# Optimization experiments

Hardware: AMD Instinct MI355X
Metric: run time of the kernel (lower is better)

## Reference

```python
import jax, jax.numpy as jnp
import numpy as np

N = 100000      # nodes
E = 3200000     # edges (avg degree 32)
F_IN = 512      # num_features
H = 256         # hidden
C = 64          # num_classes
K = 20          # APPNP propagation steps
ALPHA = 0.1     # teleport probability


def setup_inputs() -> dict:
    key = jax.random.key(0)
    k0, k1, k2, k3 = jax.random.split(key, 4)
    x = jax.random.normal(k0, (N, F_IN), dtype=jnp.float32)
    edge_index = jax.random.randint(k1, (2, E), 0, N, dtype=jnp.int64)
    W1 = jax.random.normal(k2, (F_IN, H), dtype=jnp.float32) / np.sqrt(F_IN).astype(np.float32)
    b1 = jnp.zeros((H,), jnp.float32)
    W2 = jax.random.normal(k3, (H, C), dtype=jnp.float32) / np.sqrt(H).astype(np.float32)
    b2 = jnpp = jnp.zeros((C,), jnp.float32)
    return {"x": x, "edge_index": edge_index, "W1": W1, "b1": b1, "W2": W2, "b2": b2}


def reference(x, edge_index, W1, b1, W2, b2):
    n = x.shape[0]
    # MLP encoder (dropout is identity in eval mode)
    h = jax.nn.relu(x @ W1 + b1) @ W2 + b2            # [N, C]

    # gcn_norm with added self-loops (PyG APPNP default)
    self_loop = jnp.arange(n, dtype=edge_index.dtype)
    src = jnp.concatenate([edge_index[0], self_loop])  # message sources
    dst = jnp.concatenate([edge_index[1], self_loop])  # aggregation targets
    deg = jax.ops.segment_sum(jnp.ones_like(dst, jnp.float32), dst, num_segments=n)
    deg_inv_sqrt = jnp.where(deg > 0, jax.lax.rsqrt(deg), 0.0)
    norm = (deg_inv_sqrt[src] * deg_inv_sqrt[dst])[:, None]  # [E+N, 1]

    def prop_step(_, z):
        msg = z[src] * norm                               # gather + scale
        agg = jax.ops.segment_sum(msg, dst, num_segments=n)  # scatter-add
        return (1.0 - ALPHA) * agg + ALPHA * h            # teleport mix

    z = jax.lax.fori_loop(0, K, prop_step, h)
    return jax.nn.log_softmax(z, axis=1)
```

## Files before the change

### kernel.cpp

```cpp
#include <hip/hip_runtime.h>
#include <hip/hip_bf16.h>
#include <math.h>

#define NN 100000
#define EE 3200000
#define FIN 512
#define HID 256
#define CLS 64
#define KST 20

typedef __attribute__((ext_vector_type(8))) short bf16x8;
typedef __attribute__((ext_vector_type(4))) float f32x4;

__device__ __forceinline__ short f2bf(float f) {
    union { __hip_bfloat16 b; short s; } u;
    u.b = __float2bfloat16(f);
    return u.s;
}
__device__ __forceinline__ float bf2f(__hip_bfloat16 b) { return __bfloat162float(b); }
__device__ __forceinline__ float lobf(unsigned u) { return __uint_as_float(u << 16); }
__device__ __forceinline__ float hibf(unsigned u) { return __uint_as_float(u & 0xffff0000u); }
__device__ __forceinline__ unsigned packbf(float lo, float hi) {
    return (unsigned)(unsigned short)f2bf(lo) | ((unsigned)(unsigned short)f2bf(hi) << 16);
}


__global__ void zero_kernel(int* __restrict__ degcnt, int* __restrict__ cursor) {
    int i = blockIdx.x * 256 + threadIdx.x;
    if (i < NN) { degcnt[i] = 0; cursor[i] = 0; }
}

__global__ void count_kernel(const int* __restrict__ edst, int* __restrict__ degcnt) {
    int e = blockIdx.x * 256 + threadIdx.x;
    if (e < EE) atomicAdd(&degcnt[edst[e]], 1);
}

__global__ __launch_bounds__(1024) void scan1_kernel(const int* __restrict__ degcnt,
                                                     int* __restrict__ tmp,
                                                     int* __restrict__ bsum) {
    __shared__ int s[1024];
    int t = threadIdx.x;
    int i = blockIdx.x * 1024 + t;
    int v = (i < NN) ? degcnt[i] : 0;
    s[t] = v;
    __syncthreads();
    for (int off = 1; off < 1024; off <<= 1) {
        int xv = (t >= off) ? s[t - off] : 0;
        __syncthreads();
        s[t] += xv;
        __syncthreads();
    }
    if (i < NN) tmp[i] = s[t] - v;
    if (t == 1023) bsum[blockIdx.x] = s[1023];
}

__global__ void scan2_kernel(const int* __restrict__ bsum, int* __restrict__ boff, int nb) {
    if (blockIdx.x == 0 && threadIdx.x == 0) {
        int run = 0;
        for (int b = 0; b < nb; ++b) { boff[b] = run; run += bsum[b]; }
    }
}

__global__ void finalize_kernel(const int* __restrict__ tmp, const int* __restrict__ boff,
                                const int* __restrict__ degcnt,
                                int* __restrict__ rowptr, float* __restrict__ dis) {
    int i = blockIdx.x * 256 + threadIdx.x;
    if (i < NN) {
        rowptr[i] = tmp[i] + boff[i >> 10];
        dis[i] = rsqrtf((float)(degcnt[i] + 1));
        if (i == 0) rowptr[NN] = EE;
    }
}

__global__ void fill_kernel(const int* __restrict__ esrc, const int* __restrict__ edst,
                            const int* __restrict__ rowptr, int* __restrict__ cursor,
                            int* __restrict__ csrc) {
    int e = blockIdx.x * 256 + threadIdx.x;
    if (e < EE) {
        int d = edst[e];
        int pos = atomicAdd(&cursor[d], 1);
        csrc[rowptr[d] + pos] = esrc[e];
    }
}


__global__ void w1t_kernel(const float* __restrict__ W1, __hip_bfloat16* __restrict__ W1Tt) {
    const int c = threadIdx.x;
    const int kg = blockIdx.x;
    bf16x8 o;
#pragma unroll
    for (int j = 0; j < 8; ++j) o[j] = f2bf(W1[(size_t)(kg * 8 + j) * HID + c]);
    size_t dst = ((size_t)((c >> 4) * 16 + (kg >> 2))) * 512 + (c & 15) * 32 + (kg & 3) * 8;
    *(bf16x8*)((short*)W1Tt + dst) = o;
}

__global__ void w2t_kernel(const float* __restrict__ W2, __hip_bfloat16* __restrict__ W2Tt) {
    const int c = threadIdx.x;
    const int kg = blockIdx.x;
    bf16x8 o;
#pragma unroll
    for (int j = 0; j < 8; ++j) o[j] = f2bf(W2[(size_t)(kg * 8 + j) * CLS + c]);
    size_t dst = ((size_t)((c >> 4) * 8 + (kg >> 2))) * 512 + (c & 15) * 32 + (kg & 3) * 8;
    *(bf16x8*)((short*)W2Tt + dst) = o;
}


__global__ __launch_bounds__(256, 3) void mlp_kernel(const float* __restrict__ x,
                                                     const __hip_bfloat16* __restrict__ W1Tt,
                                                     const float* __restrict__ b1,
                                                     const __hip_bfloat16* __restrict__ W2Tt,
                                                     const float* __restrict__ b2,
                                                     const float* __restrict__ dis,
                                                     __hip_bfloat16* __restrict__ hb,
                                                     __hip_bfloat16* __restrict__ y0) {
    __shared__ __align__(16) char Alds[64 * 256];
    __shared__ __align__(16) char Tlds[64 * 512];

    const int t = threadIdx.x;
    const int w = t >> 6;
    const int lane = t & 63;
    const int lg = lane >> 4;
    const int li = lane & 15;
    const int loff = li * 32 + lg * 8;
    const int r0 = blockIdx.x * 64;

    const short* W1s = (const short*)W1Tt;
    const short* W2s = (const short*)W2Tt;

    const float* xp[8];
    int srow[8], sc4[8];
#pragma unroll
    for (int i = 0; i < 8; ++i) {
        int f = t + i * 256;
        srow[i] = f >> 5;
        sc4[i] = (f & 31) << 2;
        int sr = r0 + srow[i]; if (sr >= NN) sr = NN - 1;
        xp[i] = x + (size_t)sr * FIN + sc4[i];
    }

    float4 av[8];
#pragma unroll
    for (int i = 0; i < 8; ++i) av[i] = *(const float4*)(xp[i]);

    f32x4 acc1[4][4];
#pragma unroll
    for (int mf = 0; mf < 4; ++mf)
#pragma unroll
        for (int nf = 0; nf < 4; ++nf)
#pragma unroll
            for (int r = 0; r < 4; ++r) acc1[mf][nf][r] = 0.f;

    for (int kc = 0; kc < 4; ++kc) {
#pragma unroll
        for (int i = 0; i < 8; ++i) {
            short4 b;
            b.x = f2bf(av[i].x); b.y = f2bf(av[i].y); b.z = f2bf(av[i].z); b.w = f2bf(av[i].w);
            int byte = srow[i] * 256 + ((sc4[i] * 2) ^ ((srow[i] & 7) << 4));
            *(short4*)(Alds + byte) = b;
        }
        asm volatile("s_waitcnt lgkmcnt(0)" ::: "memory");
        __builtin_amdgcn_s_barrier();
        asm volatile("" ::: "memory");

        if (kc < 3) {
#pragma unroll
            for (int i = 0; i < 8; ++i) av[i] = *(const float4*)(xp[i] + (kc + 1) * 128);
        }

#pragma unroll
        for (int ks = 0; ks < 4; ++ks) {
            bf16x8 af[4], bfw[4];
#pragma unroll
            for (int mf = 0; mf < 4; ++mf) {
                int row = mf * 16 + li;
                int kb = (ks * 32 + lg * 8) * 2;
                af[mf] = *(const bf16x8*)(Alds + row * 256 + (kb ^ ((row & 7) << 4)));
            }
#pragma unroll
            for (int nf = 0; nf < 4; ++nf)
                bfw[nf] = *(const bf16x8*)(W1s + ((size_t)((w * 4 + nf) * 16 + kc * 4 + ks)) * 512 + loff);
#pragma unroll
            for (int mf = 0; mf < 4; ++mf)
#pragma unroll
                for (int nf = 0; nf < 4; ++nf)
                    acc1[mf][nf] = __builtin_amdgcn_mfma_f32_16x16x32_bf16(
                        af[mf], bfw[nf], acc1[mf][nf], 0, 0, 0);
        }
        asm volatile("" ::: "memory");
        __builtin_amdgcn_s_barrier();
        asm volatile("" ::: "memory");
    }

#pragma unroll
    for (int nf = 0; nf < 4; ++nf) {
        const float bv = b1[w * 64 + nf * 16 + li];
        const int col = w * 64 + nf * 16 + li;
#pragma unroll
        for (int mf = 0; mf < 4; ++mf) {
#pragma unroll
            for (int r = 0; r < 4; ++r) {
                int row = mf * 16 + lg * 4 + r;
                float tv = fmaxf(acc1[mf][nf][r] + bv, 0.f);
                int byte = row * 512 + ((col * 2) ^ ((row & 7) << 4));
                *(short*)(Tlds + byte) = f2bf(tv);
            }
        }
    }
    __syncthreads();

    f32x4 acc2[4];
#pragma unroll
    for (int nf = 0; nf < 4; ++nf)
#pragma unroll
        for (int r = 0; r < 4; ++r) acc2[nf][r] = 0.f;

#pragma unroll
    for (int kt2 = 0; kt2 < 8; ++kt2) {
        int row = w * 16 + li;
        int kb = (kt2 * 32 + lg * 8) * 2;
        bf16x8 at = *(const bf16x8*)(Tlds + row * 512 + (kb ^ ((row & 7) << 4)));
#pragma unroll
        for (int nf = 0; nf < 4; ++nf) {
            bf16x8 bw = *(const bf16x8*)(W2s + ((size_t)(nf * 8 + kt2)) * 512 + loff);
            acc2[nf] = __builtin_amdgcn_mfma_f32_16x16x32_bf16(at, bw, acc2[nf], 0, 0, 0);
        }
    }

#pragma unroll
    for (int r = 0; r < 4; ++r) {
        int row = r0 + w * 16 + lg * 4 + r;
        if (row < NN) {
            const float dv = dis[row];
#pragma unroll
            for (int nf = 0; nf < 4; ++nf) {
                float hv = acc2[nf][r] + b2[nf * 16 + li];
                size_t o = (size_t)row * CLS + nf * 16 + li;
                hb[o] = __float2bfloat16(hv);
                y0[o] = __float2bfloat16(hv * dv);
            }
        }
    }
}

__device__ __forceinline__ void acc8(float* a, uint4 d) {
    a[0] += lobf(d.x); a[1] += hibf(d.x);
    a[2] += lobf(d.y); a[3] += hibf(d.y);
    a[4] += lobf(d.z); a[5] += hibf(d.z);
    a[6] += lobf(d.w); a[7] += hibf(d.w);
}

template <int LAST>
__global__ __launch_bounds__(256) void prop_kernel(const __hip_bfloat16* __restrict__ yin,
                                                   const __hip_bfloat16* __restrict__ hb,
                                                   const float* __restrict__ dis,
                                                   const int* __restrict__ rowptr,
                                                   const int* __restrict__ csrc,
                                                   __hip_bfloat16* __restrict__ yout,
                                                   float* __restrict__ zout) {
    const int node = blockIdx.x * 4 + (threadIdx.x >> 6);
    const int lane = threadIdx.x & 63;
    const int g = lane >> 3;
    const int ci = lane & 7;

    const uint4* Y = (const uint4*)yin;

    int p = __builtin_amdgcn_readfirstlane(rowptr[node]);
    const int e = __builtin_amdgcn_readfirstlane(rowptr[node + 1]);

    float a[8];
#pragma unroll
    for (int j = 0; j < 8; ++j) a[j] = 0.f;

    for (; p + 32 <= e; p += 32) {
        int s0 = csrc[p + g];
        int s1 = csrc[p + 8 + g];
        int s2 = csrc[p + 16 + g];
        int s3 = csrc[p + 24 + g];
        uint4 d0 = Y[(size_t)s0 * 8 + ci];
        uint4 d1 = Y[(size_t)s1 * 8 + ci];
        uint4 d2 = Y[(size_t)s2 * 8 + ci];
        uint4 d3 = Y[(size_t)s3 * 8 + ci];
        acc8(a, d0); acc8(a, d1); acc8(a, d2); acc8(a, d3);
    }
    for (; p + 8 <= e; p += 8) {
        int s = csrc[p + g];
        uint4 d = Y[(size_t)s * 8 + ci];
        acc8(a, d);
    }
    if (p < e) {
        int q = p + g;
        int s = csrc[(q < e) ? q : (e - 1)];
        uint4 d = Y[(size_t)s * 8 + ci];
        if (q < e) acc8(a, d);
    }

#pragma unroll
    for (int j = 0; j < 8; ++j) {
        a[j] += __shfl_xor(a[j], 8);
        a[j] += __shfl_xor(a[j], 16);
        a[j] += __shfl_xor(a[j], 32);
    }

    const float din = dis[node];
    uint4 dself = Y[(size_t)node * 8 + ci];
    uint4 dh = ((const uint4*)hb)[(size_t)node * 8 + ci];
    float sv[8], hv[8], z[8];
    acc8(a, dself);
    sv[0] = 0.f;
    (void)sv;
    hv[0] = lobf(dh.x); hv[1] = hibf(dh.x);
    hv[2] = lobf(dh.y); hv[3] = hibf(dh.y);
    hv[4] = lobf(dh.z); hv[5] = hibf(dh.z);
    hv[6] = lobf(dh.w); hv[7] = hibf(dh.w);
#pragma unroll
    for (int j = 0; j < 8; ++j) z[j] = 0.9f * din * a[j] + 0.1f * hv[j];

    if (LAST) {
        float m = z[0];
#pragma unroll
        for (int j = 1; j < 8; ++j) m = fmaxf(m, z[j]);
        m = fmaxf(m, __shfl_xor(m, 1));
        m = fmaxf(m, __shfl_xor(m, 2));
        m = fmaxf(m, __shfl_xor(m, 4));
        float ss = 0.f;
#pragma unroll
        for (int j = 0; j < 8; ++j) ss += __expf(z[j] - m);
        ss += __shfl_xor(ss, 1);
        ss += __shfl_xor(ss, 2);
        ss += __shfl_xor(ss, 4);
        const float lg = __logf(ss);
        if (g == 0) {
            float4 o0, o1;
            o0.x = z[0] - m - lg; o0.y = z[1] - m - lg; o0.z = z[2] - m - lg; o0.w = z[3] - m - lg;
            o1.x = z[4] - m - lg; o1.y = z[5] - m - lg; o1.z = z[6] - m - lg; o1.w = z[7] - m - lg;
            ((float4*)zout)[(size_t)node * 16 + ci * 2] = o0;
            ((float4*)zout)[(size_t)node * 16 + ci * 2 + 1] = o1;
        }
    } else {
        if (g == 0) {
            uint4 o;
            o.x = packbf(z[0] * din, z[1] * din);
            o.y = packbf(z[2] * din, z[3] * din);
            o.z = packbf(z[4] * din, z[5] * din);
            o.w = packbf(z[6] * din, z[7] * din);
            ((uint4*)yout)[(size_t)node * 8 + ci] = o;
        }
    }
}

extern "C" void kernel_launch(void* const* d_in, const int* in_sizes, int n_in,
                              void* d_out, int out_size, void* d_ws, size_t ws_size,
                              hipStream_t stream) {
    const float* x  = (const float*)d_in[0];
    const int*   ei = (const int*)d_in[1];
    const float* W1 = (const float*)d_in[2];
    const float* b1 = (const float*)d_in[3];
    const float* W2 = (const float*)d_in[4];
    const float* b2 = (const float*)d_in[5];
    float* out = (float*)d_out;

    const int* esrc = ei;
    const int* edst = ei + EE;

    char* w = (char*)d_ws;
    auto alloc = [&](size_t bytes) {
        char* p = w;
        w += (bytes + 255) & ~(size_t)255;
        return p;
    };
    __hip_bfloat16* hb   = (__hip_bfloat16*)alloc((size_t)NN * CLS * 2);
    __hip_bfloat16* yA   = (__hip_bfloat16*)alloc((size_t)NN * CLS * 2);
    __hip_bfloat16* yB   = (__hip_bfloat16*)alloc((size_t)NN * CLS * 2);
    __hip_bfloat16* W1Tt = (__hip_bfloat16*)alloc((size_t)HID * FIN * 2);
    __hip_bfloat16* W2Tt = (__hip_bfloat16*)alloc((size_t)CLS * HID * 2);
    float* dis   = (float*)alloc((size_t)NN * 4);
    int* degcnt  = (int*)alloc((size_t)NN * 4);
    int* tmp     = (int*)alloc((size_t)NN * 4);
    int* rowptr  = (int*)alloc((size_t)(NN + 1) * 4);
    int* cursor  = (int*)alloc((size_t)NN * 4);
    int* csrc    = (int*)alloc((size_t)EE * 4);
    int* bsum    = (int*)alloc(128 * 4);
    int* boff    = (int*)alloc(128 * 4);

    const int nbN = (NN + 255) / 256;
    const int nbE = (EE + 255) / 256;
    const int nscan = (NN + 1023) / 1024;

    zero_kernel<<<nbN, 256, 0, stream>>>(degcnt, cursor);
    count_kernel<<<nbE, 256, 0, stream>>>(edst, degcnt);
    scan1_kernel<<<nscan, 1024, 0, stream>>>(degcnt, tmp, bsum);
    scan2_kernel<<<1, 64, 0, stream>>>(bsum, boff, nscan);
    finalize_kernel<<<nbN, 256, 0, stream>>>(tmp, boff, degcnt, rowptr, dis);
    fill_kernel<<<nbE, 256, 0, stream>>>(esrc, edst, rowptr, cursor, csrc);

    w1t_kernel<<<FIN / 8, HID, 0, stream>>>(W1, W1Tt);
    w2t_kernel<<<HID / 8, CLS, 0, stream>>>(W2, W2Tt);

    mlp_kernel<<<(NN + 63) / 64, 256, 0, stream>>>(x, W1Tt, b1, W2Tt, b2, dis, hb, yA);

    const __hip_bfloat16* yin = yA;
    __hip_bfloat16* yout = yB;
    for (int s = 0; s < KST - 1; ++s) {
        prop_kernel<0><<<NN / 4, 256, 0, stream>>>(yin, hb, dis, rowptr, csrc, yout, nullptr);
        const __hip_bfloat16* t2 = yin;
        yin = yout;
        yout = (__hip_bfloat16*)t2;
    }
    prop_kernel<1><<<NN / 4, 256, 0, stream>>>(yin, hb, dis, rowptr, csrc, nullptr, out);
}
```

Measured before the change: 1.549 ms.

## Build CSR via two-level bucketed counting sort instead of global atomics

Replaces the zero/count/scan/finalize/fill CSR construction with a two-pass bucket sort. Edges are first binned by destination block of 1024 nodes using LDS atomics plus one global atomic per bucket per block. A per-bucket kernel then builds the histogram, rowptr, degree norms and the csrc fill entirely in shared memory. This removes the global atomic contention and random scattered writes across the 3.2M edges. In exchange it adds a fixed-capacity bucket buffer (BCAP) that would overflow on skewed degree distributions, and the csr stage runs on only 98 blocks.

```diff
diff --git a/kernel.cpp b/kernel.cpp
--- a/kernel.cpp
+++ b/kernel.cpp
@@ -8,6 +8,8 @@
 #define HID 256
 #define CLS 64
 #define KST 20
+#define NBUK 98
+#define BCAP 36864
 
 typedef __attribute__((ext_vector_type(8))) short bf16x8;
 typedef __attribute__((ext_vector_type(4))) float f32x4;
@@ -25,61 +27,110 @@
 }
 
 
-__global__ void zero_kernel(int* __restrict__ degcnt, int* __restrict__ cursor) {
-    int i = blockIdx.x * 256 + threadIdx.x;
-    if (i < NN) { degcnt[i] = 0; cursor[i] = 0; }
-}
-
-__global__ void count_kernel(const int* __restrict__ edst, int* __restrict__ degcnt) {
-    int e = blockIdx.x * 256 + threadIdx.x;
-    if (e < EE) atomicAdd(&degcnt[edst[e]], 1);
-}
-
-__global__ __launch_bounds__(1024) void scan1_kernel(const int* __restrict__ degcnt,
-                                                     int* __restrict__ tmp,
-                                                     int* __restrict__ bsum) {
-    __shared__ int s[1024];
-    int t = threadIdx.x;
-    int i = blockIdx.x * 1024 + t;
-    int v = (i < NN) ? degcnt[i] : 0;
-    s[t] = v;
-    __syncthreads();
-    for (int off = 1; off < 1024; off <<= 1) {
-        int xv = (t >= off) ? s[t - off] : 0;
+__global__ void zerocur_kernel(int* __restrict__ gcur) {
+    if (threadIdx.x < NBUK) gcur[threadIdx.x] = 0;
+}
+
+__global__ __launch_bounds__(256) void bucket_kernel(const int* __restrict__ esrc,
+                                                     const int* __restrict__ edst,
+                                                     unsigned* __restrict__ gbuf,
+                                                     int* __restrict__ gcur) {
+    __shared__ int lcnt[NBUK];
+    __shared__ int lbase[NBUK];
+    const int t = threadIdx.x;
+    for (int i = t; i < NBUK; i += 256) lcnt[i] = 0;
+    __syncthreads();
+
+    const int e0 = blockIdx.x * 2048;
+    int bkt[8], rnk[8];
+    unsigned rec[8];
+#pragma unroll
+    for (int i = 0; i < 8; ++i) {
+        int idx = e0 + i * 256 + t;
+        if (idx < EE) {
+            int d = edst[idx];
+            int s = esrc[idx];
+            bkt[i] = d >> 10;
+            rec[i] = ((unsigned)(d & 1023) << 17) | (unsigned)s;
+            rnk[i] = atomicAdd(&lcnt[bkt[i]], 1);
+        } else {
+            bkt[i] = -1;
+        }
+    }
+    __syncthreads();
+    for (int i = t; i < NBUK; i += 256) lbase[i] = atomicAdd(&gcur[i], lcnt[i]);
+    __syncthreads();
+#pragma unroll
+    for (int i = 0; i < 8; ++i)
+        if (bkt[i] >= 0)
+            gbuf[(size_t)bkt[i] * BCAP + lbase[bkt[i]] + rnk[i]] = rec[i];
+}
+
+__global__ void prefix_kernel(const int* __restrict__ gcur, int* __restrict__ bb,
+                              int* __restrict__ rowptr) {
+    if (threadIdx.x == 0) {
+        int run = 0;
+        for (int b = 0; b < NBUK; ++b) { bb[b] = run; run += gcur[b]; }
+        bb[NBUK] = run;
+        rowptr[NN] = run;
+    }
+}
+
+__global__ __launch_bounds__(256) void csr_kernel(const unsigned* __restrict__ gbuf,
+                                                  const int* __restrict__ gcur,
+                                                  const int* __restrict__ bb,
+                                                  int* __restrict__ rowptr,
+                                                  float* __restrict__ dis,
+                                                  int* __restrict__ csrc) {
+    __shared__ int hist[1024];
+    __shared__ int part[256];
+    __shared__ int rp[1024];
+    const int b = blockIdx.x;
+    const int t = threadIdx.x;
+    const int d0 = b << 10;
+    const int nrec = gcur[b];
+    const unsigned* rbuf = gbuf + (size_t)b * BCAP;
+    const int base = bb[b];
+
+#pragma unroll
+    for (int i = 0; i < 4; ++i) hist[t * 4 + i] = 0;
+    __syncthreads();
+    for (int r = t; r < nrec; r += 256)
+        atomicAdd(&hist[rbuf[r] >> 17], 1);
+    __syncthreads();
+
+    int h[4], sum4 = 0;
+#pragma unroll
+    for (int i = 0; i < 4; ++i) { h[i] = hist[t * 4 + i]; sum4 += h[i]; }
+    part[t] = sum4;
+    __syncthreads();
+    for (int off = 1; off < 256; off <<= 1) {
+        int v = (t >= off) ? part[t - off] : 0;
         __syncthreads();
-        s[t] += xv;
+        part[t] += v;
         __syncthreads();
     }
-    if (i < NN) tmp[i] = s[t] - v;
-    if (t == 1023) bsum[blockIdx.x] = s[1023];
-}
-
-__global__ void scan2_kernel(const int* __restrict__ bsum, int* __restrict__ boff, int nb) {
-    if (blockIdx.x == 0 && threadIdx.x == 0) {
-        int run = 0;
-        for (int b = 0; b < nb; ++b) { boff[b] = run; run += bsum[b]; }
-    }
-}
-
-__global__ void finalize_kernel(const int* __restrict__ tmp, const int* __restrict__ boff,
-                                const int* __restrict__ degcnt,
-                                int* __restrict__ rowptr, float* __restrict__ dis) {
-    int i = blockIdx.x * 256 + threadIdx.x;
-    if (i < NN) {
-        rowptr[i] = tmp[i] + boff[i >> 10];
-        dis[i] = rsqrtf((float)(degcnt[i] + 1));
-        if (i == 0) rowptr[NN] = EE;
-    }
-}
-
-__global__ void fill_kernel(const int* __restrict__ esrc, const int* __restrict__ edst,
-                            const int* __restrict__ rowptr, int* __restrict__ cursor,
-                            int* __restrict__ csrc) {
-    int e = blockIdx.x * 256 + threadIdx.x;
-    if (e < EE) {
-        int d = edst[e];
-        int pos = atomicAdd(&cursor[d], 1);
-        csrc[rowptr[d] + pos] = esrc[e];
+
+    int run = base + part[t] - sum4;
+#pragma unroll
+    for (int i = 0; i < 4; ++i) {
+        int d = d0 + t * 4 + i;
+        if (d < NN) {
+            rowptr[d] = run;
+            rp[t * 4 + i] = run;
+            dis[d] = rsqrtf((float)(h[i] + 1));
+        }
+        run += h[i];
+    }
+#pragma unroll
+    for (int i = 0; i < 4; ++i) hist[t * 4 + i] = 0;
+    __syncthreads();
+
+    for (int r = t; r < nrec; r += 256) {
+        unsigned rec = rbuf[r];
+        int dloc = rec >> 17;
+        int pos = atomicAdd(&hist[dloc], 1);
+        csrc[rp[dloc] + pos] = (int)(rec & 0x1FFFFu);
     }
 }
 
@@ -241,6 +292,7 @@
         }
     }
 }
+
 
 __device__ __forceinline__ void acc8(float* a, uint4 d) {
     a[0] += lobf(d.x); a[1] += hibf(d.x);
@@ -304,10 +356,8 @@
     const float din = dis[node];
     uint4 dself = Y[(size_t)node * 8 + ci];
     uint4 dh = ((const uint4*)hb)[(size_t)node * 8 + ci];
-    float sv[8], hv[8], z[8];
+    float hv[8], z[8];
     acc8(a, dself);
-    sv[0] = 0.f;
-    (void)sv;
     hv[0] = lobf(dh.x); hv[1] = hibf(dh.x);
     hv[2] = lobf(dh.y); hv[3] = hibf(dh.y);
     hv[4] = lobf(dh.z); hv[5] = hibf(dh.z);
@@ -328,11 +378,11 @@
         ss += __shfl_xor(ss, 1);
         ss += __shfl_xor(ss, 2);
         ss += __shfl_xor(ss, 4);
-        const float lg = __logf(ss);
+        const float lgv = __logf(ss);
         if (g == 0) {
             float4 o0, o1;
-            o0.x = z[0] - m - lg; o0.y = z[1] - m - lg; o0.z = z[2] - m - lg; o0.w = z[3] - m - lg;
-            o1.x = z[4] - m - lg; o1.y = z[5] - m - lg; o1.z = z[6] - m - lg; o1.w = z[7] - m - lg;
+            o0.x = z[0] - m - lgv; o0.y = z[1] - m - lgv; o0.z = z[2] - m - lgv; o0.w = z[3] - m - lgv;
+            o1.x = z[4] - m - lgv; o1.y = z[5] - m - lgv; o1.z = z[6] - m - lgv; o1.w = z[7] - m - lgv;
             ((float4*)zout)[(size_t)node * 16 + ci * 2] = o0;
             ((float4*)zout)[(size_t)node * 16 + ci * 2 + 1] = o1;
         }
@@ -373,29 +423,20 @@
     __hip_bfloat16* yB   = (__hip_bfloat16*)alloc((size_t)NN * CLS * 2);
     __hip_bfloat16* W1Tt = (__hip_bfloat16*)alloc((size_t)HID * FIN * 2);
     __hip_bfloat16* W2Tt = (__hip_bfloat16*)alloc((size_t)CLS * HID * 2);
-    float* dis   = (float*)alloc((size_t)NN * 4);
-    int* degcnt  = (int*)alloc((size_t)NN * 4);
-    int* tmp     = (int*)alloc((size_t)NN * 4);
-    int* rowptr  = (int*)alloc((size_t)(NN + 1) * 4);
-    int* cursor  = (int*)alloc((size_t)NN * 4);
-    int* csrc    = (int*)alloc((size_t)EE * 4);
-    int* bsum    = (int*)alloc(128 * 4);
-    int* boff    = (int*)alloc(128 * 4);
-
-    const int nbN = (NN + 255) / 256;
-    const int nbE = (EE + 255) / 256;
-    const int nscan = (NN + 1023) / 1024;
-
-    zero_kernel<<<nbN, 256, 0, stream>>>(degcnt, cursor);
-    count_kernel<<<nbE, 256, 0, stream>>>(edst, degcnt);
-    scan1_kernel<<<nscan, 1024, 0, stream>>>(degcnt, tmp, bsum);
-    scan2_kernel<<<1, 64, 0, stream>>>(bsum, boff, nscan);
-    finalize_kernel<<<nbN, 256, 0, stream>>>(tmp, boff, degcnt, rowptr, dis);
-    fill_kernel<<<nbE, 256, 0, stream>>>(esrc, edst, rowptr, cursor, csrc);
+    float* dis    = (float*)alloc((size_t)NN * 4);
+    int* rowptr   = (int*)alloc((size_t)(NN + 1) * 4);
+    int* csrc     = (int*)alloc((size_t)EE * 4);
+    unsigned* gbuf = (unsigned*)alloc((size_t)NBUK * BCAP * 4);
+    int* gcur     = (int*)alloc(NBUK * 4);
+    int* bb       = (int*)alloc((NBUK + 1) * 4);
+
+    zerocur_kernel<<<1, 128, 0, stream>>>(gcur);
+    bucket_kernel<<<(EE + 2047) / 2048, 256, 0, stream>>>(esrc, edst, gbuf, gcur);
+    prefix_kernel<<<1, 64, 0, stream>>>(gcur, bb, rowptr);
+    csr_kernel<<<NBUK, 256, 0, stream>>>(gbuf, gcur, bb, rowptr, dis, csrc);
 
     w1t_kernel<<<FIN / 8, HID, 0, stream>>>(W1, W1Tt);
     w2t_kernel<<<HID / 8, CLS, 0, stream>>>(W2, W2Tt);
-
     mlp_kernel<<<(NN + 63) / 64, 256, 0, stream>>>(x, W1Tt, b1, W2Tt, b2, dis, hb, yA);
 
     const __hip_bfloat16* yin = yA;
```

Measured after the change: 1.375 ms. 11.3% less time.
